# Optimization experiments

Measured on AMD Instinct MI355X. Metric: run time of the kernel, lower is better.

Reference implementation:

```python
import jax, jax.numpy as jnp
import numpy as np

HIDDEN = 128
N_NODES = 50000
N_EDGES = 640000


def setup_inputs() -> dict:
    key = jax.random.key(0)
    k1, k2, k3, k4, k5, k6, k7 = jax.random.split(key, 7)
    z = jax.random.normal(k1, (N_NODES, HIDDEN), dtype=jnp.float32)
    edge_index = jax.random.randint(k2, (2, N_EDGES), 0, N_NODES, dtype=jnp.int64)
    # Linear params (torch default uniform(-1/sqrt(fan_in), 1/sqrt(fan_in)))
    b1 = 1.0 / np.sqrt(2 * HIDDEN)
    W1 = jax.random.uniform(k3, (HIDDEN, 2 * HIDDEN), jnp.float32, -b1, b1)
    bias1 = jax.random.uniform(k4, (HIDDEN,), jnp.float32, -b1, b1)
    b2 = 1.0 / np.sqrt(HIDDEN)
    W2 = jax.random.uniform(k5, (1, HIDDEN), jnp.float32, -b2, b2)
    bias2 = jax.random.uniform(k6, (1,), jnp.float32, -b2, b2)
    return {"z": z, "W1": W1, "bias1": bias1, "W2": W2, "bias2": bias2,
            "edge_index": edge_index}


def reference(z, W1, bias1, W2, bias2, edge_index):
    # Gather endpoint embeddings: [E, H] each
    z_src = z[edge_index[0]]
    z_dst = z[edge_index[1]]
    h = jnp.concatenate([z_src, z_dst], axis=-1)  # [E, 2H]
    h = jax.nn.relu(h @ W1.T + bias1)             # [E, H]
    out = h @ W2.T + bias2                        # [E, 1]
    return out.reshape(-1)
```

## Files before the change

### kernel.cpp

```cpp
#include <hip/hip_runtime.h>
#include <hip/hip_bf16.h>


#define N_NODES 50000
#define N_EDGES 640000
#define H 128

using bf16 = __hip_bfloat16;
typedef __attribute__((ext_vector_type(8))) short short8;
typedef __attribute__((ext_vector_type(4))) float f32x4;

#define GLD_LDS16(g, l)                                                     \
  __builtin_amdgcn_global_load_lds(                                         \
      (const __attribute__((address_space(1))) void*)(g),                   \
      (__attribute__((address_space(3))) void*)(l), 16, 0, 0)

static __device__ __forceinline__ short bfbits(float x) {
  __hip_bfloat16 h = __float2bfloat16(x);
  return *reinterpret_cast<short*>(&h);
}

static __device__ __forceinline__ short8 pack8(float4 a, float4 b) {
  short8 r;
  r[0] = bfbits(a.x); r[1] = bfbits(a.y); r[2] = bfbits(a.z); r[3] = bfbits(a.w);
  r[4] = bfbits(b.x); r[5] = bfbits(b.y); r[6] = bfbits(b.z); r[7] = bfbits(b.w);
  return r;
}

__global__ __launch_bounds__(256) void w_to_bf16(const float* __restrict__ W1,
                                                 bf16* __restrict__ Wb) {
  const int u = blockIdx.x * 256 + threadIdx.x;
  const int o = u >> 4, k8 = (u & 15) * 8;
  const float4* src = reinterpret_cast<const float4*>(
      W1 + (size_t)(o & (H - 1)) * (2 * H) + (o >> 7) * H + k8);
  *reinterpret_cast<short8*>(Wb + (size_t)o * H + k8) = pack8(src[0], src[1]);
}

#define HP 136

__global__ __launch_bounds__(256) void precompute_uv(
    const float* __restrict__ z, const bf16* __restrict__ Wb,
    const float* __restrict__ bias1, bf16* __restrict__ U,
    bf16* __restrict__ V) {
  __shared__ float ldsF[32 * H];
  __shared__ bf16 ldsH[32 * HP];
  const int tid = threadIdx.x;
  const int lane = tid & 63;
  const int s = tid >> 6;
  const int l15 = lane & 15, quad = lane >> 4;
  const int nodebase = blockIdx.x * 32;

  {
    int r0 = nodebase + s * 8;
    if (r0 > N_NODES - 8) r0 = N_NODES - 8;
    const float* gsrc = z + (size_t)r0 * H + lane * 4;
    float* ldst = ldsF + s * 8 * H;
#pragma unroll
    for (int j = 0; j < 4; ++j) GLD_LDS16(gsrc + j * 256, ldst + j * 256);
  }

  short8 wf[4][4];
#pragma unroll
  for (int t = 0; t < 4; ++t) {
    const bf16* wp = Wb + (size_t)(s * 64 + t * 16 + l15) * H + quad * 8;
#pragma unroll
    for (int q = 0; q < 4; ++q)
      wf[t][q] = *reinterpret_cast<const short8*>(wp + q * 32);
  }

  __syncthreads();

  {
    const int row = tid >> 3, off = (tid & 7) * 16;
    const float4* fp = reinterpret_cast<const float4*>(ldsF + row * H + off);
    const float4 a = fp[0], b = fp[1], c = fp[2], d = fp[3];
    *reinterpret_cast<short8*>(&ldsH[row * HP + off]) = pack8(a, b);
    *reinterpret_cast<short8*>(&ldsH[row * HP + off + 8]) = pack8(c, d);
  }
  __syncthreads();

  short8 zf[2][4];
#pragma unroll
  for (int m = 0; m < 2; ++m)
#pragma unroll
    for (int q = 0; q < 4; ++q)
      zf[m][q] = *reinterpret_cast<const short8*>(
          &ldsH[(m * 16 + l15) * HP + quad * 8 + q * 32]);

  f32x4 acc[2][4] = {};
#pragma unroll
  for (int m = 0; m < 2; ++m)
#pragma unroll
    for (int t = 0; t < 4; ++t)
#pragma unroll
      for (int q = 0; q < 4; ++q)
        acc[m][t] =
            __builtin_amdgcn_mfma_f32_16x16x32_bf16(wf[t][q], zf[m][q], acc[m][t], 0, 0, 0);

  bf16* epi = reinterpret_cast<bf16*>(ldsF);
#pragma unroll
  for (int m = 0; m < 2; ++m) {
    const int nl = m * 16 + l15;
#pragma unroll
    for (int t = 0; t < 4; ++t) {
      const int o = s * 64 + t * 16 + quad * 4;
      const float4 bv = *reinterpret_cast<const float4*>(bias1 + (o & (H - 1)));
      ushort4 st;
      st.x = (unsigned short)bfbits(acc[m][t][0] + 0.5f * bv.x);
      st.y = (unsigned short)bfbits(acc[m][t][1] + 0.5f * bv.y);
      st.z = (unsigned short)bfbits(acc[m][t][2] + 0.5f * bv.z);
      st.w = (unsigned short)bfbits(acc[m][t][3] + 0.5f * bv.w);
      *reinterpret_cast<ushort4*>(epi + nl * 256 + o) = st;
    }
  }
  __syncthreads();

#pragma unroll
  for (int half = 0; half < 2; ++half) {
    bf16* base = half ? V : U;
#pragma unroll
    for (int it = 0; it < 2; ++it) {
      const int nl = s * 8 + it * 4 + (lane >> 4);
      const int oc = (lane & 15) * 8;
      const short8 v = *reinterpret_cast<const short8*>(epi + nl * 256 + half * H + oc);
      const int n = nodebase + nl;
      if (n < N_NODES)
        *reinterpret_cast<short8*>(base + (size_t)n * H + oc) = v;
    }
  }
}

static __device__ __forceinline__ void acc2(unsigned u, unsigned v,
                                            float w2lo, float w2hi, float& sum) {
  const float ulo = __uint_as_float(u << 16);
  const float uhi = __uint_as_float(u & 0xffff0000u);
  const float vlo = __uint_as_float(v << 16);
  const float vhi = __uint_as_float(v & 0xffff0000u);
  float h0 = fmaxf(ulo + vlo, 0.f);
  float h1 = fmaxf(uhi + vhi, 0.f);
  sum = fmaf(h0, w2lo, sum);
  sum = fmaf(h1, w2hi, sum);
}

__global__ __launch_bounds__(256, 4) void edge_decode(
    const int* __restrict__ eidx, const bf16* __restrict__ Ub,
    const bf16* __restrict__ Vb, const float* __restrict__ W2,
    const float* __restrict__ bias2, float* __restrict__ out) {
  const int lane = threadIdx.x & 63;
  const int e8 = lane & 7;

  float w2r[16];
  const float4* wp = reinterpret_cast<const float4*>(W2 + e8 * 16);
#pragma unroll
  for (int q = 0; q < 4; ++q) {
    const float4 wv = wp[q];
    w2r[q * 4 + 0] = wv.x; w2r[q * 4 + 1] = wv.y;
    w2r[q * 4 + 2] = wv.z; w2r[q * 4 + 3] = wv.w;
  }
  const float b2 = bias2[0];

  const uint4* U4 = reinterpret_cast<const uint4*>(Ub);
  const uint4* V4 = reinterpret_cast<const uint4*>(Vb);

  const int wid0 = blockIdx.x * 4 + (int)(threadIdx.x >> 6);
  for (int c = wid0; c < N_EDGES / 64; c += 4096) {
    const int chunk = c * 64;
    const int src = eidx[chunk + lane];
    const int dst = eidx[N_EDGES + chunk + lane];

    float res = 0.f;
#pragma unroll
    for (int half = 0; half < 2; ++half) {
      uint4 ua[4], ub[4], va[4], vb[4];
#pragma unroll
      for (int j = 0; j < 4; ++j) {
        const int i = half * 4 + j;
        const int sl = (lane & 56) | i;
        const int s_i = __shfl(src, sl);
        const int d_i = __shfl(dst, sl);
        const uint4* up = U4 + (size_t)s_i * 16 + e8 * 2;
        const uint4* vp = V4 + (size_t)d_i * 16 + e8 * 2;
        ua[j] = up[0]; ub[j] = up[1];
        va[j] = vp[0]; vb[j] = vp[1];
      }
      __builtin_amdgcn_sched_barrier(0);
#pragma unroll
      for (int j = 0; j < 4; ++j) {
        const int i = half * 4 + j;
        float sum = 0.f;
        acc2(ua[j].x, va[j].x, w2r[0],  w2r[1],  sum);
        acc2(ua[j].y, va[j].y, w2r[2],  w2r[3],  sum);
        acc2(ua[j].z, va[j].z, w2r[4],  w2r[5],  sum);
        acc2(ua[j].w, va[j].w, w2r[6],  w2r[7],  sum);
        acc2(ub[j].x, vb[j].x, w2r[8],  w2r[9],  sum);
        acc2(ub[j].y, vb[j].y, w2r[10], w2r[11], sum);
        acc2(ub[j].z, vb[j].z, w2r[12], w2r[13], sum);
        acc2(ub[j].w, vb[j].w, w2r[14], w2r[15], sum);
        sum += __shfl_xor(sum, 1);
        sum += __shfl_xor(sum, 2);
        sum += __shfl_xor(sum, 4);
        if (e8 == i) res = sum + b2;
      }
    }
    out[chunk + lane] = res;
  }
}

extern "C" void kernel_launch(void* const* d_in, const int* in_sizes, int n_in,
                              void* d_out, int out_size, void* d_ws, size_t ws_size,
                              hipStream_t stream) {
  const float* z     = (const float*)d_in[0];
  const float* W1    = (const float*)d_in[1];
  const float* bias1 = (const float*)d_in[2];
  const float* W2    = (const float*)d_in[3];
  const float* bias2 = (const float*)d_in[4];
  const int*   eidx  = (const int*)d_in[5];
  float* out = (float*)d_out;

  bf16* U  = (bf16*)d_ws;
  bf16* V  = U + (size_t)N_NODES * H;
  bf16* Wb = V + (size_t)N_NODES * H;

  hipLaunchKernelGGL(w_to_bf16, dim3(16), dim3(256), 0, stream, W1, Wb);
  hipLaunchKernelGGL(precompute_uv, dim3((N_NODES + 31) / 32), dim3(256), 0,
                     stream, z, Wb, bias1, U, V);
  hipLaunchKernelGGL(edge_decode, dim3(1024), dim3(256), 0, stream,
                     eidx, U, V, W2, bias2, out);
}
```

Baseline: 139.1 us.

## Bucket-sort edges by source node to improve gather locality in edge decode

Adds a binning pass that groups edges into 196 buckets by the source node's high bits, plus a per-bucket counting sort on the low byte. Edge decode then walks the sorted lists, so consecutive warps read nearby U rows and get better cache reuse, and results scatter back to their original edge ids. The W1 conversion is folded into the binning launch. This costs extra kernels, a memset, atomics and a scattered output write, and it relies on node ids fitting in 16 bits and on an overflow path when a bucket fills.

```diff
diff --git a/kernel.cpp b/kernel.cpp
--- a/kernel.cpp
+++ b/kernel.cpp
@@ -5,6 +5,13 @@
 #define N_NODES 50000
 #define N_EDGES 640000
 #define H 128
+
+#define NBUK 196
+#define CAP 3840
+#define CHUNKS 15
+#define BIN_BLOCKS 128
+#define EPT 20
+#define OVF_MAX 65536
 
 using bf16 = __hip_bfloat16;
 typedef __attribute__((ext_vector_type(8))) short short8;
@@ -25,15 +32,6 @@
   r[0] = bfbits(a.x); r[1] = bfbits(a.y); r[2] = bfbits(a.z); r[3] = bfbits(a.w);
   r[4] = bfbits(b.x); r[5] = bfbits(b.y); r[6] = bfbits(b.z); r[7] = bfbits(b.w);
   return r;
-}
-
-__global__ __launch_bounds__(256) void w_to_bf16(const float* __restrict__ W1,
-                                                 bf16* __restrict__ Wb) {
-  const int u = blockIdx.x * 256 + threadIdx.x;
-  const int o = u >> 4, k8 = (u & 15) * 8;
-  const float4* src = reinterpret_cast<const float4*>(
-      W1 + (size_t)(o & (H - 1)) * (2 * H) + (o >> 7) * H + k8);
-  *reinterpret_cast<short8*>(Wb + (size_t)o * H + k8) = pack8(src[0], src[1]);
 }
 
 #define HP 136
@@ -130,6 +128,108 @@
   }
 }
 
+__global__ __launch_bounds__(256) void bin196(
+    const int* __restrict__ eidx, const float* __restrict__ W1,
+    bf16* __restrict__ Wb, int* __restrict__ cursors, int* __restrict__ ovfn,
+    unsigned long long* __restrict__ buk,
+    unsigned long long* __restrict__ ovfl) {
+  if (blockIdx.x >= BIN_BLOCKS) {
+    const int u = (blockIdx.x - BIN_BLOCKS) * 256 + threadIdx.x;
+    const int o = u >> 4, k8 = (u & 15) * 8;
+    const float4* src = reinterpret_cast<const float4*>(
+        W1 + (size_t)(o & (H - 1)) * (2 * H) + (o >> 7) * H + k8);
+    *reinterpret_cast<short8*>(Wb + (size_t)o * H + k8) = pack8(src[0], src[1]);
+    return;
+  }
+  __shared__ int lh[256];
+  __shared__ int lcur[256];
+  const int t = threadIdx.x;
+  lh[t] = 0;
+  __syncthreads();
+  unsigned long long ent[EPT];
+  int key[EPT];
+  const int base = blockIdx.x * (256 * EPT) + t;
+#pragma unroll
+  for (int j = 0; j < EPT; ++j) {
+    const int e = base + j * 256;
+    if (e < N_EDGES) {
+      const unsigned s = (unsigned)eidx[e];
+      const unsigned d = (unsigned)eidx[N_EDGES + e];
+      ent[j] = ((unsigned long long)(unsigned)e << 32) | (d << 16) | s;
+      key[j] = (int)(s >> 8);
+      atomicAdd(&lh[key[j]], 1);
+    } else {
+      key[j] = -1;
+    }
+  }
+  __syncthreads();
+  lcur[t] = lh[t] ? atomicAdd(&cursors[t * 16], lh[t]) : 0;
+  __syncthreads();
+#pragma unroll
+  for (int j = 0; j < EPT; ++j) {
+    if (key[j] >= 0) {
+      const int pos = atomicAdd(&lcur[key[j]], 1);
+      if (pos < CAP) {
+        buk[(size_t)key[j] * CAP + pos] = ent[j];
+      } else {
+        const int op = atomicAdd(ovfn, 1);
+        if (op < OVF_MAX) ovfl[op] = ent[j];
+      }
+    }
+  }
+}
+
+__global__ __launch_bounds__(256) void bsort(
+    int* __restrict__ cursors, unsigned long long* __restrict__ buk) {
+  __shared__ int hist[256];
+  __shared__ int cur[256];
+  const int t = threadIdx.x;
+  const int b = blockIdx.x;
+  const int n = min(cursors[b * 16], CAP);
+  unsigned long long* g = buk + (size_t)b * CAP;
+
+  hist[t] = 0;
+  __syncthreads();
+
+  unsigned long long ent[CHUNKS];
+  int key[CHUNKS];
+#pragma unroll
+  for (int j = 0; j < CHUNKS; ++j) {
+    const int i = t + j * 256;
+    if (i < n) {
+      ent[j] = g[i];
+      key[j] = (int)(ent[j] & 0xffu);
+      atomicAdd(&hist[key[j]], 1);
+    } else {
+      key[j] = -1;
+    }
+  }
+  __syncthreads();
+
+  const int c = hist[t];
+  int incl = c;
+  __syncthreads();
+  hist[t] = incl;
+  for (int off = 1; off < 256; off <<= 1) {
+    __syncthreads();
+    const int add = (t >= off) ? hist[t - off] : 0;
+    __syncthreads();
+    incl += add;
+    hist[t] = incl;
+  }
+  __syncthreads();
+  cur[t] = incl - c;
+  __syncthreads();
+
+#pragma unroll
+  for (int j = 0; j < CHUNKS; ++j) {
+    if (key[j] >= 0) {
+      const int pos = atomicAdd(&cur[key[j]], 1);
+      g[pos] = ent[j];
+    }
+  }
+}
+
 static __device__ __forceinline__ void acc2(unsigned u, unsigned v,
                                             float w2lo, float w2hi, float& sum) {
   const float ulo = __uint_as_float(u << 16);
@@ -142,12 +242,61 @@
   sum = fmaf(h1, w2hi, sum);
 }
 
+static __device__ __forceinline__ void decode64(
+    const unsigned long long* __restrict__ ents, int mvalid,
+    const uint4* __restrict__ U4, const uint4* __restrict__ V4,
+    const float* w2r, float b2, float* __restrict__ out, int lane, int e8) {
+  const bool valid = lane < mvalid;
+  const unsigned long long v = valid ? ents[lane] : 0ull;
+  const int src = (int)(v & 0xffffu);
+  const int dst = (int)((v >> 16) & 0xffffu);
+  const int eid = (int)(v >> 32);
+
+  float res = 0.f;
+#pragma unroll
+  for (int half = 0; half < 2; ++half) {
+    uint4 ua[4], ub[4], va[4], vb[4];
+#pragma unroll
+    for (int j = 0; j < 4; ++j) {
+      const int i = half * 4 + j;
+      const int sl = (lane & 56) | i;
+      const int s_i = __shfl(src, sl);
+      const int d_i = __shfl(dst, sl);
+      const uint4* up = U4 + (size_t)s_i * 16 + e8 * 2;
+      const uint4* vp = V4 + (size_t)d_i * 16 + e8 * 2;
+      ua[j] = up[0]; ub[j] = up[1];
+      va[j] = vp[0]; vb[j] = vp[1];
+    }
+#pragma unroll
+    for (int j = 0; j < 4; ++j) {
+      const int i = half * 4 + j;
+      float sum = 0.f;
+      acc2(ua[j].x, va[j].x, w2r[0],  w2r[1],  sum);
+      acc2(ua[j].y, va[j].y, w2r[2],  w2r[3],  sum);
+      acc2(ua[j].z, va[j].z, w2r[4],  w2r[5],  sum);
+      acc2(ua[j].w, va[j].w, w2r[6],  w2r[7],  sum);
+      acc2(ub[j].x, vb[j].x, w2r[8],  w2r[9],  sum);
+      acc2(ub[j].y, vb[j].y, w2r[10], w2r[11], sum);
+      acc2(ub[j].z, vb[j].z, w2r[12], w2r[13], sum);
+      acc2(ub[j].w, vb[j].w, w2r[14], w2r[15], sum);
+      sum += __shfl_xor(sum, 1);
+      sum += __shfl_xor(sum, 2);
+      sum += __shfl_xor(sum, 4);
+      if (e8 == i) res = sum + b2;
+    }
+  }
+  if (valid) out[eid] = res;
+}
+
 __global__ __launch_bounds__(256, 4) void edge_decode(
-    const int* __restrict__ eidx, const bf16* __restrict__ Ub,
-    const bf16* __restrict__ Vb, const float* __restrict__ W2,
-    const float* __restrict__ bias2, float* __restrict__ out) {
+    const unsigned long long* __restrict__ buk, const int* __restrict__ cursors,
+    const int* __restrict__ ovfn, const unsigned long long* __restrict__ ovfl,
+    const bf16* __restrict__ Ub, const bf16* __restrict__ Vb,
+    const float* __restrict__ W2, const float* __restrict__ bias2,
+    float* __restrict__ out) {
   const int lane = threadIdx.x & 63;
   const int e8 = lane & 7;
+  const int w = threadIdx.x >> 6;
 
   float w2r[16];
   const float4* wp = reinterpret_cast<const float4*>(W2 + e8 * 16);
@@ -162,48 +311,17 @@
   const uint4* U4 = reinterpret_cast<const uint4*>(Ub);
   const uint4* V4 = reinterpret_cast<const uint4*>(Vb);
 
-  const int wid0 = blockIdx.x * 4 + (int)(threadIdx.x >> 6);
-  for (int c = wid0; c < N_EDGES / 64; c += 4096) {
-    const int chunk = c * 64;
-    const int src = eidx[chunk + lane];
-    const int dst = eidx[N_EDGES + chunk + lane];
-
-    float res = 0.f;
-#pragma unroll
-    for (int half = 0; half < 2; ++half) {
-      uint4 ua[4], ub[4], va[4], vb[4];
-#pragma unroll
-      for (int j = 0; j < 4; ++j) {
-        const int i = half * 4 + j;
-        const int sl = (lane & 56) | i;
-        const int s_i = __shfl(src, sl);
-        const int d_i = __shfl(dst, sl);
-        const uint4* up = U4 + (size_t)s_i * 16 + e8 * 2;
-        const uint4* vp = V4 + (size_t)d_i * 16 + e8 * 2;
-        ua[j] = up[0]; ub[j] = up[1];
-        va[j] = vp[0]; vb[j] = vp[1];
-      }
-      __builtin_amdgcn_sched_barrier(0);
-#pragma unroll
-      for (int j = 0; j < 4; ++j) {
-        const int i = half * 4 + j;
-        float sum = 0.f;
-        acc2(ua[j].x, va[j].x, w2r[0],  w2r[1],  sum);
-        acc2(ua[j].y, va[j].y, w2r[2],  w2r[3],  sum);
-        acc2(ua[j].z, va[j].z, w2r[4],  w2r[5],  sum);
-        acc2(ua[j].w, va[j].w, w2r[6],  w2r[7],  sum);
-        acc2(ub[j].x, vb[j].x, w2r[8],  w2r[9],  sum);
-        acc2(ub[j].y, vb[j].y, w2r[10], w2r[11], sum);
-        acc2(ub[j].z, vb[j].z, w2r[12], w2r[13], sum);
-        acc2(ub[j].w, vb[j].w, w2r[14], w2r[15], sum);
-        sum += __shfl_xor(sum, 1);
-        sum += __shfl_xor(sum, 2);
-        sum += __shfl_xor(sum, 4);
-        if (e8 == i) res = sum + b2;
-      }
-    }
-    out[chunk + lane] = res;
-  }
+  const int b = blockIdx.x / CHUNKS;
+  const int k = blockIdx.x - b * CHUNKS;
+  const int n = min(cursors[b * 16], CAP);
+  const int base = k * 256 + w * 64;
+  if (base < n)
+    decode64(buk + (size_t)b * CAP + base, min(64, n - base), U4, V4, w2r, b2,
+             out, lane, e8);
+
+  const int no = min(*ovfn, OVF_MAX);
+  for (int b0 = (blockIdx.x * 4 + w) * 64; b0 < no; b0 += (int)gridDim.x * 4 * 64)
+    decode64(ovfl + b0, min(64, no - b0), U4, V4, w2r, b2, out, lane, e8);
 }
 
 extern "C" void kernel_launch(void* const* d_in, const int* in_sizes, int n_in,
@@ -220,10 +338,20 @@
   bf16* U  = (bf16*)d_ws;
   bf16* V  = U + (size_t)N_NODES * H;
   bf16* Wb = V + (size_t)N_NODES * H;
-
-  hipLaunchKernelGGL(w_to_bf16, dim3(16), dim3(256), 0, stream, W1, Wb);
+  unsigned long long* buk =
+      (unsigned long long*)(Wb + 256 * H);
+  int* cursors = (int*)(buk + (size_t)NBUK * CAP);
+  int* ovfn    = cursors + NBUK * 16;
+  unsigned long long* ovfl =
+      (unsigned long long*)(cursors + NBUK * 16 + 16);
+
+  hipMemsetAsync(cursors, 0, (NBUK * 16 + 16) * sizeof(int), stream);
+
+  hipLaunchKernelGGL(bin196, dim3(BIN_BLOCKS + 16), dim3(256), 0, stream,
+                     eidx, W1, Wb, cursors, ovfn, buk, ovfl);
+  hipLaunchKernelGGL(bsort, dim3(NBUK), dim3(256), 0, stream, cursors, buk);
   hipLaunchKernelGGL(precompute_uv, dim3((N_NODES + 31) / 32), dim3(256), 0,
                      stream, z, Wb, bias1, U, V);
-  hipLaunchKernelGGL(edge_decode, dim3(1024), dim3(256), 0, stream,
-                     eidx, U, V, W2, bias2, out);
-}
+  hipLaunchKernelGGL(edge_decode, dim3(NBUK * CHUNKS), dim3(256), 0, stream,
+                     buk, cursors, ovfn, ovfl, U, V, W2, bias2, out);
+}
```

After: 152.7 us. +9.8%, slower.
